# Performance work log

Measured on AMD Instinct MI355X. Metric: run time of the kernel, lower is better.

Reference implementation:

```python
import jax, jax.numpy as jnp
import numpy as np

LAT_SIZE = 2048
BATCH = 4096


def cos_pos_encoding_1d(size, freq_div=2.0, sub_freq_max=4.0):
    freqs = list(range(1, int(size / freq_div)))
    spaces = [np.linspace(0, freq * 2 * np.pi, size) for freq in freqs]
    sub_freqs = [1.0 / float(i) for i in range(2, int(sub_freq_max))]
    sub_spaces = [np.linspace(i * freq * 2 * np.pi, (i + 1) * freq * 2 * np.pi, size)
                  for freq in sub_freqs for i in range(int(1 / freq))]
    spaces = spaces + sub_spaces
    cos = [np.cos(space) for space in spaces]
    return np.stack(cos).astype(np.float32)  # (n_freq, size)


def setup_inputs() -> dict:
    key = jax.random.key(0)
    k1, k2 = jax.random.split(key)
    cos_basis = jnp.asarray(cos_pos_encoding_1d(LAT_SIZE, 1, 8))  # (2074, 2048)
    n_freq = cos_basis.shape[0]
    x = jax.random.normal(k1, (BATCH, LAT_SIZE), dtype=jnp.float32)
    # nn.Linear default init: U(-1/sqrt(in), 1/sqrt(in))
    bound = 1.0 / np.sqrt(LAT_SIZE)
    W = jax.random.uniform(k2, (n_freq, LAT_SIZE), dtype=jnp.float32,
                           minval=-bound, maxval=bound)
    return {"x": x, "W": W, "cos_basis": cos_basis}


def reference(x, W, cos_basis):
    # x: (B, lat), W: (n_freq, lat), cos_basis: (n_freq, lat)
    x_freqs = x @ W.T                          # (B, n_freq)  -- to_freq_size
    # broadcast-mul + sum over freq dim == GEMM against fixed cosine basis
    out = x_freqs @ cos_basis                  # (B, lat)
    # global max-normalize (norm=True)
    return out / jnp.max(out)
```

## Files before the change

### kernel.cpp

```cpp
#include <hip/hip_runtime.h>
#include <hip/hip_bf16.h>
#include <cstdint>

#define BATCH 4096
#define LAT   2048
#define NFREQ 2074
#define KPAD  2112

typedef __bf16 bf16x8 __attribute__((ext_vector_type(8)));
typedef float  f32x4  __attribute__((ext_vector_type(4)));

__device__ __forceinline__ unsigned short f2bf(float f) {
    unsigned int u = __float_as_uint(f);
    u = (u + 0x7fffu + ((u >> 16) & 1u)) >> 16;
    return (unsigned short)u;
}

__device__ __forceinline__ void gload_lds16(const unsigned short* g, unsigned short* l) {
    __builtin_amdgcn_global_load_lds(
        (const __attribute__((address_space(1))) unsigned int*)g,
        (__attribute__((address_space(3))) unsigned int*)l,
        16, 0, 0);
}


__global__ void prep_kernel(const float* __restrict__ W,
                            const float* __restrict__ cb,
                            unsigned short* __restrict__ WT,
                            unsigned short* __restrict__ cosT,
                            float* __restrict__ maxp) {
    __shared__ float t[64][65];
    const int bid = blockIdx.x;
    const int tid = threadIdx.x;
    if (bid == 0 && tid == 0) *maxp = -__builtin_inff();
    const float* in     = (bid < 1056) ? W  : cb;
    unsigned short* out = (bid < 1056) ? WT : cosT;
    int b2 = (bid < 1056) ? bid : bid - 1056;
    const int c0 = (b2 % 32) * 64;
    const int r0 = (b2 / 32) * 64;
    for (int i = tid; i < 1024; i += 256) {
        int rr = i >> 4;
        int c4 = (i & 15) * 4;
        int r  = r0 + rr;
        float4 v;
        if (r < NFREQ) v = *(const float4*)&in[(size_t)r * LAT + c0 + c4];
        else           v = make_float4(0.f, 0.f, 0.f, 0.f);
        t[rr][c4 + 0] = v.x; t[rr][c4 + 1] = v.y;
        t[rr][c4 + 2] = v.z; t[rr][c4 + 3] = v.w;
    }
    __syncthreads();
    for (int i = tid; i < 1024; i += 256) {
        int cc = i >> 4;
        int r4 = (i & 15) * 4;
        ushort4 o;
        o.x = f2bf(t[r4 + 0][cc]); o.y = f2bf(t[r4 + 1][cc]);
        o.z = f2bf(t[r4 + 2][cc]); o.w = f2bf(t[r4 + 3][cc]);
        *(ushort4*)&out[(size_t)(c0 + cc) * KPAD + r0 + r4] = o;
    }
}

template <int N, int K>
__global__ __launch_bounds__(512, 4)
void gemm1_kernel(const unsigned short* __restrict__ A,
                  const unsigned short* __restrict__ Bt,
                  unsigned short* __restrict__ C,
                  const float* __restrict__ x,
                  unsigned short* __restrict__ xb) {
    if (blockIdx.y >= 16) {
        const int cb  = (blockIdx.y - 16) * 16 + blockIdx.x;
        const int tid = threadIdx.x;
        const float4* x4 = (const float4*)x;
        uint4* o4 = (uint4*)xb;
        int i = cb * 512 + tid;
#pragma unroll
        for (int it = 0; it < 8; ++it, i += 131072) {
            float4 a = x4[2 * i];
            float4 b = x4[2 * i + 1];
            union { unsigned short us[8]; uint4 v; } p;
            p.us[0] = f2bf(a.x); p.us[1] = f2bf(a.y); p.us[2] = f2bf(a.z); p.us[3] = f2bf(a.w);
            p.us[4] = f2bf(b.x); p.us[5] = f2bf(b.y); p.us[6] = f2bf(b.z); p.us[7] = f2bf(b.w);
            o4[i] = p.v;
        }
        return;
    }

    __shared__ alignas(16) unsigned short As[3][128 * 32];
    __shared__ alignas(16) unsigned short Bs[3][128 * 32];

    const int tid  = threadIdx.x;
    const int wave = tid >> 6;
    const int lane = tid & 63;
    const int wm   = (wave >> 2) * 64;
    const int wn   = (wave & 3) * 32;
    const int quad = lane >> 4;
    const int l16  = lane & 15;

    const int mBase = blockIdx.y * 128;
    const int nBase = blockIdx.x * 128;

    const int srow = lane >> 2;
    const int sk   = (((lane & 3) ^ ((srow >> 1) & 3))) * 8;

    const unsigned short* Ab1 = A  + (size_t)(mBase + wave * 16 + srow) * K + sk;
    const unsigned short* Bb1 = Bt + (size_t)(nBase + wave * 16 + srow) * K + sk;
    const int coff = (wave * 16) * 32;

    const int pc = (quad ^ ((l16 >> 1) & 3)) * 8;

    constexpr int NIT = K / 32;
    gload_lds16(Ab1, &As[0][coff]);
    gload_lds16(Bb1, &Bs[0][coff]);

    f32x4 acc[4][2] = {};
    int bc = 0;
    for (int j = 0; j < NIT; ++j) {
        const int bn = (bc == 2) ? 0 : bc + 1;
        if (j + 1 < NIT) {
            const int k0 = (j + 1) * 32;
            gload_lds16(Ab1 + k0, &As[bn][coff]);
            gload_lds16(Bb1 + k0, &Bs[bn][coff]);
            asm volatile("s_waitcnt vmcnt(2)\n\ts_barrier" ::: "memory");
        } else {
            asm volatile("s_waitcnt vmcnt(0)\n\ts_barrier" ::: "memory");
        }
        bf16x8 af[4], bfr[2];
#pragma unroll
        for (int mi = 0; mi < 4; ++mi)
            af[mi] = *(const bf16x8*)&As[bc][(wm + mi * 16 + l16) * 32 + pc];
#pragma unroll
        for (int ni = 0; ni < 2; ++ni)
            bfr[ni] = *(const bf16x8*)&Bs[bc][(wn + ni * 16 + l16) * 32 + pc];
#pragma unroll
        for (int mi = 0; mi < 4; ++mi)
#pragma unroll
            for (int ni = 0; ni < 2; ++ni)
                acc[mi][ni] = __builtin_amdgcn_mfma_f32_16x16x32_bf16(
                    af[mi], bfr[ni], acc[mi][ni], 0, 0, 0);
        bc = bn;
    }

#pragma unroll
    for (int mi = 0; mi < 4; ++mi)
#pragma unroll
        for (int ni = 0; ni < 2; ++ni) {
            int col = nBase + wn + ni * 16 + l16;
#pragma unroll
            for (int r = 0; r < 4; ++r) {
                int row = mBase + wm + mi * 16 + quad * 4 + r;
                C[(size_t)row * N + col] = f2bf(acc[mi][ni][r]);
            }
        }
}

template <int N, int K>
__global__ __launch_bounds__(512, 2)
void gemm2_kernel(const unsigned short* __restrict__ A,
                  const unsigned short* __restrict__ Bt,
                  unsigned short* __restrict__ Cb,
                  float* __restrict__ maxp) {
    __shared__ alignas(16) unsigned short As[3][256 * 64];
    __shared__ alignas(16) unsigned short Bs[3][128 * 64];
    __shared__ float redbuf[8];

    const int tid  = threadIdx.x;
    const int wave = tid >> 6;
    const int lane = tid & 63;
    const int wm   = (wave >> 1) * 64;
    const int wn   = (wave & 1) * 64;
    const int quad = lane >> 4;
    const int l16  = lane & 15;

    const int mBase = blockIdx.y * 256;
    const int nBase = blockIdx.x * 128;

    const int lrow = lane >> 3;
    const int lchk = ((lane & 7) ^ lrow) * 8;
    const unsigned short* Ab = A  + (size_t)(mBase + wave * 32 + lrow) * K + lchk;
    const unsigned short* Bb = Bt + (size_t)(nBase + wave * 16 + lrow) * K + lchk;
    const int aoff = (wave * 32) * 64;
    const int boff = (wave * 16) * 64;

    const int r7  = l16 & 7;
    const int pc0 = ((0 * 4 + quad) ^ r7) * 8;
    const int pc1 = ((1 * 4 + quad) ^ r7) * 8;

    constexpr int NIT = K / 64;
#pragma unroll
    for (int d = 0; d < 4; ++d)
        gload_lds16(Ab + (size_t)(d * 8) * K, &As[0][aoff + d * 8 * 64]);
#pragma unroll
    for (int d = 0; d < 2; ++d)
        gload_lds16(Bb + (size_t)(d * 8) * K, &Bs[0][boff + d * 8 * 64]);

    f32x4 acc[4][4] = {};
    int bc = 0;
    for (int j = 0; j < NIT; ++j) {
        const int bn = (bc == 2) ? 0 : bc + 1;
        if (j + 1 < NIT) {
            const int k0 = (j + 1) * 64;
#pragma unroll
            for (int d = 0; d < 4; ++d)
                gload_lds16(Ab + (size_t)(d * 8) * K + k0, &As[bn][aoff + d * 8 * 64]);
#pragma unroll
            for (int d = 0; d < 2; ++d)
                gload_lds16(Bb + (size_t)(d * 8) * K + k0, &Bs[bn][boff + d * 8 * 64]);
            asm volatile("s_waitcnt vmcnt(6)\n\ts_barrier" ::: "memory");
        } else {
            asm volatile("s_waitcnt vmcnt(0)\n\ts_barrier" ::: "memory");
        }
        {
            bf16x8 af[4], bfr[4];
#pragma unroll
            for (int mi = 0; mi < 4; ++mi)
                af[mi] = *(const bf16x8*)&As[bc][(wm + mi * 16 + l16) * 64 + pc0];
#pragma unroll
            for (int ni = 0; ni < 4; ++ni)
                bfr[ni] = *(const bf16x8*)&Bs[bc][(wn + ni * 16 + l16) * 64 + pc0];
#pragma unroll
            for (int mi = 0; mi < 4; ++mi)
#pragma unroll
                for (int ni = 0; ni < 4; ++ni)
                    acc[mi][ni] = __builtin_amdgcn_mfma_f32_16x16x32_bf16(
                        af[mi], bfr[ni], acc[mi][ni], 0, 0, 0);
        }
        {
            bf16x8 af[4], bfr[4];
#pragma unroll
            for (int mi = 0; mi < 4; ++mi)
                af[mi] = *(const bf16x8*)&As[bc][(wm + mi * 16 + l16) * 64 + pc1];
#pragma unroll
            for (int ni = 0; ni < 4; ++ni)
                bfr[ni] = *(const bf16x8*)&Bs[bc][(wn + ni * 16 + l16) * 64 + pc1];
#pragma unroll
            for (int mi = 0; mi < 4; ++mi)
#pragma unroll
                for (int ni = 0; ni < 4; ++ni)
                    acc[mi][ni] = __builtin_amdgcn_mfma_f32_16x16x32_bf16(
                        af[mi], bfr[ni], acc[mi][ni], 0, 0, 0);
        }
        bc = bn;
    }

    float vmax = -__builtin_inff();
#pragma unroll
    for (int mi = 0; mi < 4; ++mi)
#pragma unroll
        for (int ni = 0; ni < 4; ++ni) {
            int col = nBase + wn + ni * 16 + l16;
#pragma unroll
            for (int r = 0; r < 4; ++r) {
                int row = mBase + wm + mi * 16 + quad * 4 + r;
                float v = acc[mi][ni][r];
                Cb[(size_t)row * N + col] = f2bf(v);
                vmax = fmaxf(vmax, v);
            }
        }
#pragma unroll
    for (int off = 32; off > 0; off >>= 1)
        vmax = fmaxf(vmax, __shfl_xor(vmax, off));
    if (lane == 0) redbuf[wave] = vmax;
    __syncthreads();
    if (tid == 0) {
        float m = redbuf[0];
#pragma unroll
        for (int w = 1; w < 8; ++w) m = fmaxf(m, redbuf[w]);
        if (m >= 0.0f) atomicMax((int*)maxp, __float_as_int(m));
        else           atomicMin((unsigned int*)maxp, __float_as_uint(m));
    }
}

__global__ void scale_kernel(const unsigned short* __restrict__ cbuf,
                             float* __restrict__ out,
                             const float* __restrict__ maxp) {
    int i = blockIdx.x * blockDim.x + threadIdx.x;
    float inv = 1.0f / (*maxp);
    union { uint4 v; unsigned short us[8]; } p;
    p.v = ((const uint4*)cbuf)[i];
    float4 o0, o1;
    o0.x = __uint_as_float((unsigned int)p.us[0] << 16) * inv;
    o0.y = __uint_as_float((unsigned int)p.us[1] << 16) * inv;
    o0.z = __uint_as_float((unsigned int)p.us[2] << 16) * inv;
    o0.w = __uint_as_float((unsigned int)p.us[3] << 16) * inv;
    o1.x = __uint_as_float((unsigned int)p.us[4] << 16) * inv;
    o1.y = __uint_as_float((unsigned int)p.us[5] << 16) * inv;
    o1.z = __uint_as_float((unsigned int)p.us[6] << 16) * inv;
    o1.w = __uint_as_float((unsigned int)p.us[7] << 16) * inv;
    ((float4*)out)[2 * i]     = o0;
    ((float4*)out)[2 * i + 1] = o1;
}

extern "C" void kernel_launch(void* const* d_in, const int* in_sizes, int n_in,
                              void* d_out, int out_size, void* d_ws, size_t ws_size,
                              hipStream_t stream) {
    const float* x  = (const float*)d_in[0];
    const float* W  = (const float*)d_in[1];
    const float* cb = (const float*)d_in[2];

    char* ws = (char*)d_ws;
    unsigned short* xb   = (unsigned short*)ws;
    unsigned short* WT   = (unsigned short*)(ws + (size_t)BATCH * LAT * 2);
    unsigned short* cosT = (unsigned short*)((char*)WT + (size_t)LAT * KPAD * 2);
    unsigned short* C1   = (unsigned short*)((char*)cosT + (size_t)LAT * KPAD * 2);
    unsigned short* C2b  = (unsigned short*)((char*)C1 + (size_t)LAT * LAT * 2);
    float*          maxp = (float*)((char*)C2b + (size_t)BATCH * LAT * 2);
    float*          out  = (float*)d_out;

    prep_kernel<<<2 * 1056, 256, 0, stream>>>(W, cb, WT, cosT, maxp);

    gemm1_kernel<LAT, KPAD>
        <<<dim3(16, 32), 512, 0, stream>>>(cosT, WT, C1, x, xb);

    gemm2_kernel<LAT, LAT>
        <<<dim3(LAT / 128, BATCH / 256), 512, 0, stream>>>(xb, C1, C2b, maxp);

    scale_kernel<<<(out_size / 8) / 256, 256, 0, stream>>>(C2b, out, maxp);
}
```

Before: 181.0 us.

## Restructure gemm1 to 4-wave 64x64 warp tiles with interleaved x conversion

```diff
diff --git a/kernel.cpp b/kernel.cpp
--- a/kernel.cpp
+++ b/kernel.cpp
@@ -60,89 +60,108 @@
 }
 
 template <int N, int K>
-__global__ __launch_bounds__(512, 4)
+__global__ __launch_bounds__(256, 1)
 void gemm1_kernel(const unsigned short* __restrict__ A,
                   const unsigned short* __restrict__ Bt,
                   unsigned short* __restrict__ C,
                   const float* __restrict__ x,
                   unsigned short* __restrict__ xb) {
-    if (blockIdx.y >= 16) {
-        const int cb  = (blockIdx.y - 16) * 16 + blockIdx.x;
-        const int tid = threadIdx.x;
-        const float4* x4 = (const float4*)x;
-        uint4* o4 = (uint4*)xb;
-        int i = cb * 512 + tid;
-#pragma unroll
-        for (int it = 0; it < 8; ++it, i += 131072) {
+    __shared__ alignas(16) unsigned short As[3][128 * 64];
+    __shared__ alignas(16) unsigned short Bs[3][128 * 64];
+
+    const int tid  = threadIdx.x;
+    const int wave = tid >> 6;
+    const int lane = tid & 63;
+    const int wm   = (wave >> 1) * 64;
+    const int wn   = (wave & 1) * 64;
+    const int quad = lane >> 4;
+    const int l16  = lane & 15;
+
+    const int mBase = blockIdx.y * 128;
+    const int nBase = blockIdx.x * 128;
+
+    const int lrow = lane >> 3;
+    const int lchk = ((lane & 7) ^ lrow) * 8;
+    const unsigned short* Ab = A  + (size_t)(mBase + wave * 32 + lrow) * K + lchk;
+    const unsigned short* Bb = Bt + (size_t)(nBase + wave * 32 + lrow) * K + lchk;
+    const int coff = (wave * 32) * 64;
+
+    const int r7  = l16 & 7;
+    const int pc0 = ((0 * 4 + quad) ^ r7) * 8;
+    const int pc1 = ((1 * 4 + quad) ^ r7) * 8;
+
+    const int blk = blockIdx.y * 16 + blockIdx.x;
+    const float4* x4 = (const float4*)x;
+    uint4* xo4 = (uint4*)xb;
+
+    constexpr int NIT = K / 64;
+#pragma unroll
+    for (int d = 0; d < 4; ++d) {
+        gload_lds16(Ab + (size_t)(d * 8) * K, &As[0][coff + d * 8 * 64]);
+        gload_lds16(Bb + (size_t)(d * 8) * K, &Bs[0][coff + d * 8 * 64]);
+    }
+
+    f32x4 acc[4][4] = {};
+    int bc = 0;
+    for (int j = 0; j < NIT; ++j) {
+        const int bn = (bc == 2) ? 0 : bc + 1;
+        if (j + 1 < NIT) {
+            const int k0 = (j + 1) * 64;
+#pragma unroll
+            for (int d = 0; d < 4; ++d) {
+                gload_lds16(Ab + (size_t)(d * 8) * K + k0, &As[bn][coff + d * 8 * 64]);
+                gload_lds16(Bb + (size_t)(d * 8) * K + k0, &Bs[bn][coff + d * 8 * 64]);
+            }
+            asm volatile("s_waitcnt vmcnt(8)\n\ts_barrier" ::: "memory");
+        } else {
+            asm volatile("s_waitcnt vmcnt(0)\n\ts_barrier" ::: "memory");
+        }
+        if (j >= 1 && j <= 16) {
+            int i = blk * 4096 + (j - 1) * 256 + tid;
             float4 a = x4[2 * i];
             float4 b = x4[2 * i + 1];
             union { unsigned short us[8]; uint4 v; } p;
             p.us[0] = f2bf(a.x); p.us[1] = f2bf(a.y); p.us[2] = f2bf(a.z); p.us[3] = f2bf(a.w);
             p.us[4] = f2bf(b.x); p.us[5] = f2bf(b.y); p.us[6] = f2bf(b.z); p.us[7] = f2bf(b.w);
-            o4[i] = p.v;
-        }
-        return;
-    }
-
-    __shared__ alignas(16) unsigned short As[3][128 * 32];
-    __shared__ alignas(16) unsigned short Bs[3][128 * 32];
-
-    const int tid  = threadIdx.x;
-    const int wave = tid >> 6;
-    const int lane = tid & 63;
-    const int wm   = (wave >> 2) * 64;
-    const int wn   = (wave & 3) * 32;
-    const int quad = lane >> 4;
-    const int l16  = lane & 15;
-
-    const int mBase = blockIdx.y * 128;
-    const int nBase = blockIdx.x * 128;
-
-    const int srow = lane >> 2;
-    const int sk   = (((lane & 3) ^ ((srow >> 1) & 3))) * 8;
-
-    const unsigned short* Ab1 = A  + (size_t)(mBase + wave * 16 + srow) * K + sk;
-    const unsigned short* Bb1 = Bt + (size_t)(nBase + wave * 16 + srow) * K + sk;
-    const int coff = (wave * 16) * 32;
-
-    const int pc = (quad ^ ((l16 >> 1) & 3)) * 8;
-
-    constexpr int NIT = K / 32;
-    gload_lds16(Ab1, &As[0][coff]);
-    gload_lds16(Bb1, &Bs[0][coff]);
-
-    f32x4 acc[4][2] = {};
-    int bc = 0;
-    for (int j = 0; j < NIT; ++j) {
-        const int bn = (bc == 2) ? 0 : bc + 1;
-        if (j + 1 < NIT) {
-            const int k0 = (j + 1) * 32;
-            gload_lds16(Ab1 + k0, &As[bn][coff]);
-            gload_lds16(Bb1 + k0, &Bs[bn][coff]);
-            asm volatile("s_waitcnt vmcnt(2)\n\ts_barrier" ::: "memory");
-        } else {
-            asm volatile("s_waitcnt vmcnt(0)\n\ts_barrier" ::: "memory");
-        }
-        bf16x8 af[4], bfr[2];
-#pragma unroll
-        for (int mi = 0; mi < 4; ++mi)
-            af[mi] = *(const bf16x8*)&As[bc][(wm + mi * 16 + l16) * 32 + pc];
-#pragma unroll
-        for (int ni = 0; ni < 2; ++ni)
-            bfr[ni] = *(const bf16x8*)&Bs[bc][(wn + ni * 16 + l16) * 32 + pc];
-#pragma unroll
-        for (int mi = 0; mi < 4; ++mi)
-#pragma unroll
-            for (int ni = 0; ni < 2; ++ni)
-                acc[mi][ni] = __builtin_amdgcn_mfma_f32_16x16x32_bf16(
-                    af[mi], bfr[ni], acc[mi][ni], 0, 0, 0);
+            xo4[i] = p.v;
+        }
+        {
+            bf16x8 af[4], bfr[4];
+#pragma unroll
+            for (int mi = 0; mi < 4; ++mi)
+                af[mi] = *(const bf16x8*)&As[bc][(wm + mi * 16 + l16) * 64 + pc0];
+#pragma unroll
+            for (int ni = 0; ni < 4; ++ni)
+                bfr[ni] = *(const bf16x8*)&Bs[bc][(wn + ni * 16 + l16) * 64 + pc0];
+#pragma unroll
+            for (int mi = 0; mi < 4; ++mi)
+#pragma unroll
+                for (int ni = 0; ni < 4; ++ni)
+                    acc[mi][ni] = __builtin_amdgcn_mfma_f32_16x16x32_bf16(
+                        af[mi], bfr[ni], acc[mi][ni], 0, 0, 0);
+        }
+        {
+            bf16x8 af[4], bfr[4];
+#pragma unroll
+            for (int mi = 0; mi < 4; ++mi)
+                af[mi] = *(const bf16x8*)&As[bc][(wm + mi * 16 + l16) * 64 + pc1];
+#pragma unroll
+            for (int ni = 0; ni < 4; ++ni)
+                bfr[ni] = *(const bf16x8*)&Bs[bc][(wn + ni * 16 + l16) * 64 + pc1];
+#pragma unroll
+            for (int mi = 0; mi < 4; ++mi)
+#pragma unroll
+                for (int ni = 0; ni < 4; ++ni)
+                    acc[mi][ni] = __builtin_amdgcn_mfma_f32_16x16x32_bf16(
+                        af[mi], bfr[ni], acc[mi][ni], 0, 0, 0);
+        }
         bc = bn;
     }
 
 #pragma unroll
     for (int mi = 0; mi < 4; ++mi)
 #pragma unroll
-        for (int ni = 0; ni < 2; ++ni) {
+        for (int ni = 0; ni < 4; ++ni) {
             int col = nBase + wn + ni * 16 + l16;
 #pragma unroll
             for (int r = 0; r < 4; ++r) {
@@ -308,7 +327,7 @@
     prep_kernel<<<2 * 1056, 256, 0, stream>>>(W, cb, WT, cosT, maxp);
 
     gemm1_kernel<LAT, KPAD>
-        <<<dim3(16, 32), 512, 0, stream>>>(cosT, WT, C1, x, xb);
+        <<<dim3(16, 16), 256, 0, stream>>>(cosT, WT, C1, x, xb);
 
     gemm2_kernel<LAT, LAT>
         <<<dim3(LAT / 128, BATCH / 256), 512, 0, stream>>>(xb, C1, C2b, maxp);
```

Result: slower. 186.3 us (+2.9%).
